# Kernel tuning notes

Hardware: AMD Instinct MI355X
Metric: run time of the kernel (lower is better)

Reference implementation:

```python
import jax, jax.numpy as jnp
import numpy as np

N, E, D_IN, D_OUT = 100000, 3200000, 128, 128


def setup_inputs() -> dict:
    key = jax.random.key(0)
    ks = jax.random.split(key, 6)
    return {
        "x": jax.random.normal(ks[0], (N, D_IN), dtype=jnp.float32),
        "row": jax.random.randint(ks[1], (E,), 0, N),
        "col": jax.random.randint(ks[2], (E,), 0, N),
        "W0": jax.random.normal(ks[3], (D_OUT, D_IN), dtype=jnp.float32) * (1.0 / np.sqrt(D_IN)),
        "b0": jnp.zeros((D_OUT,), jnp.float32),
        "W1": jax.random.normal(ks[4], (D_OUT, D_IN), dtype=jnp.float32) * (1.0 / np.sqrt(D_IN)),
        "b1": jnp.zeros((D_OUT,), jnp.float32),
        "att": jax.random.normal(ks[5], (2 * D_OUT,), dtype=jnp.float32) * 0.1,
        "scale0": jnp.ones((D_OUT,), jnp.float32),
        "offset0": jnp.zeros((D_OUT,), jnp.float32),
        "scale1": jnp.ones((D_OUT,), jnp.float32),
        "offset1": jnp.zeros((D_OUT,), jnp.float32),
    }


def _norm(f, scale, offset):
    # per-node normalization over feature dim (bias='norm' branch)
    m = jnp.mean(f, axis=1, keepdims=True)
    v = jnp.var(f, axis=1, keepdims=True) + 1e-9
    return (f - m) * scale * jax.lax.rsqrt(v) + offset


def reference(x, row, col, W0, b0, W1, b1, att, scale0, offset0, scale1, offset1):
    d = W0.shape[0]
    # order-0 (self) and order-1 (neighbor) feature transforms, act='relu'
    h0 = jax.nn.relu(x @ W0.T + b0)  # [N, d]
    h1 = jax.nn.relu(x @ W1.T + b1)  # [N, d]
    # unnormalized GAT attention (no softmax), LeakyReLU(0.2)
    a_self = jax.nn.leaky_relu(h0 @ att[:d], negative_slope=0.2)   # [N]
    a_neigh = jax.nn.leaky_relu(h1 @ att[d:], negative_slope=0.2)  # [N]
    e = a_self[row] + a_neigh[col]                                 # [E]
    # SpMM: out[i] = sum_{(i,j) in edges} e_ij * h1[j]
    agg = jax.ops.segment_sum(e[:, None] * h1[col], row, num_segments=h0.shape[0])
    # batch-norm style normalization per head, then mean-aggregate over orders
    out = _norm(h0, scale0, offset0) + _norm(agg, scale1, offset1)
    return out
```

## Files before the change

### kernel.cpp

```cpp
#include <hip/hip_runtime.h>
#include <hip/hip_bf16.h>

constexpr int D = 128;
constexpr int BUCKET_SHIFT = 6;
constexpr int BUCKET_CAP_LOG2 = 12;
constexpr int BUCKET_CAP = 1 << BUCKET_CAP_LOG2;
constexpr int SEG_SHIFT = 13;
constexpr int NSEG = 13;
constexpr int BINS_PER_BUCKET = 4 * NSEG * 16;
constexpr int BINS_PER_WAVE = NSEG * 16;
constexpr int ROWSTRIDE = 130;
typedef __hip_bfloat16 bf16;
typedef __attribute__((ext_vector_type(8))) short bf16x8;
typedef __attribute__((ext_vector_type(4))) float f32x4;

__device__ __forceinline__ short f2b(float f) {
  bf16 h = __float2bfloat16(f);
  return *reinterpret_cast<short*>(&h);
}

__global__ void k_cvtW(const float* __restrict__ W0, const float* __restrict__ W1,
                       short* __restrict__ Wb0, short* __restrict__ Wb1)
{
  int i = blockIdx.x * 256 + threadIdx.x;
  if (i < 16384) Wb0[i] = f2b(W0[i]);
  else if (i < 32768) { int j = i - 16384; Wb1[j] = f2b(W1[j]); }
}

__global__ __launch_bounds__(256) void k_gemm(
    const float* __restrict__ x,
    const short* __restrict__ Wb0, const float* __restrict__ b0,
    const short* __restrict__ Wb1, const float* __restrict__ b1,
    const float* __restrict__ att,
    float* __restrict__ h0, bf16* __restrict__ h1b,
    float* __restrict__ a_self, float* __restrict__ a_neigh, int N)
{
  const int t = threadIdx.x;
  const int wv = t >> 6;
  const int l = t & 63;
  const int fb = blockIdx.y;
  const int nbase = blockIdx.x * 64 + wv * 16;
  const int lm = l & 15;
  const int lk = l >> 4;

  const short* __restrict__ W    = fb ? Wb1 : Wb0;
  const float* __restrict__ bias = fb ? b1 : b0;
  const float* __restrict__ attp = att + fb * 128;

  f32x4 acc[8];
#pragma unroll
  for (int i = 0; i < 8; ++i) acc[i] = (f32x4){0.f, 0.f, 0.f, 0.f};

  const int node_a = nbase + lm;
  const bool okA = node_a < N;
  const float* xrow = x + (size_t)node_a * D + lk * 8;

#pragma unroll
  for (int ks = 0; ks < 4; ++ks) {
    float4 a0, a1;
    if (okA) {
      a0 = *reinterpret_cast<const float4*>(xrow + ks * 32);
      a1 = *reinterpret_cast<const float4*>(xrow + ks * 32 + 4);
    } else {
      a0 = make_float4(0.f, 0.f, 0.f, 0.f);
      a1 = a0;
    }
    bf16x8 af;
    af[0] = f2b(a0.x); af[1] = f2b(a0.y); af[2] = f2b(a0.z); af[3] = f2b(a0.w);
    af[4] = f2b(a1.x); af[5] = f2b(a1.y); af[6] = f2b(a1.z); af[7] = f2b(a1.w);
#pragma unroll
    for (int nt = 0; nt < 8; ++nt) {
      const bf16x8 bfr = *reinterpret_cast<const bf16x8*>(
          W + (size_t)(nt * 16 + lm) * D + ks * 32 + lk * 8);
      acc[nt] = __builtin_amdgcn_mfma_f32_16x16x32_bf16(af, bfr, acc[nt], 0, 0, 0);
    }
  }

  float pd[4] = {0.f, 0.f, 0.f, 0.f};
#pragma unroll
  for (int nt = 0; nt < 8; ++nt) {
    const int f = nt * 16 + lm;
    const float bv = bias[f];
    const float av = attp[f];
#pragma unroll
    for (int j = 0; j < 4; ++j) {
      const float r = fmaxf(acc[nt][j] + bv, 0.f);
      pd[j] = fmaf(r, av, pd[j]);
      const int ng = nbase + lk * 4 + j;
      if (ng < N) {
        if (fb == 0) h0[(size_t)ng * D + f] = r;
        else         h1b[(size_t)ng * D + f] = __float2bfloat16(r);
      }
    }
  }
#pragma unroll
  for (int m2 = 1; m2 < 16; m2 <<= 1) {
    pd[0] += __shfl_xor(pd[0], m2, 16);
    pd[1] += __shfl_xor(pd[1], m2, 16);
    pd[2] += __shfl_xor(pd[2], m2, 16);
    pd[3] += __shfl_xor(pd[3], m2, 16);
  }
  if (lm == 0) {
    float* __restrict__ adest = fb ? a_neigh : a_self;
#pragma unroll
    for (int j = 0; j < 4; ++j) {
      const int ng = nbase + lk * 4 + j;
      if (ng < N) adest[ng] = pd[j];
    }
  }
}

__global__ __launch_bounds__(512) void k_binA(
    const int* __restrict__ row, const int* __restrict__ col,
    int* __restrict__ bukCnt, unsigned* __restrict__ buf1, int E, int NBUK)
{
  constexpr int EPB = 16384;
  __shared__ int hist[1600];
  __shared__ int base[1600];
  const int t = threadIdx.x;
  const int e0 = blockIdx.x * EPB;
  const int e1 = min(e0 + EPB, E);

  for (int i = t; i < NBUK; i += 512) hist[i] = 0;
  __syncthreads();
  for (int e = e0 + t; e < e1; e += 512)
    atomicAdd(&hist[row[e] >> BUCKET_SHIFT], 1);
  __syncthreads();
  for (int bk = t; bk < NBUK; bk += 512) {
    int c = hist[bk];
    base[bk] = (c > 0) ? atomicAdd(&bukCnt[bk], c) : 0;
  }
  __syncthreads();
  for (int i = t; i < NBUK; i += 512) hist[i] = 0;
  __syncthreads();
  for (int e = e0 + t; e < e1; e += 512) {
    int r = row[e];
    int c = col[e];
    int bk = r >> BUCKET_SHIFT;
    int pos = base[bk] + atomicAdd(&hist[bk], 1);
    if (pos < BUCKET_CAP)
      buf1[((size_t)bk << BUCKET_CAP_LOG2) + pos] =
          ((unsigned)c << BUCKET_SHIFT) | (unsigned)(r & 63);
  }
}

__global__ __launch_bounds__(1024) void k_scanB(
    const int* __restrict__ bukCnt, int* __restrict__ bukBase,
    int* __restrict__ runs, int NBUK)
{
  __shared__ int sd[1024];
  __shared__ int carry;
  const int t = threadIdx.x;
  if (t == 0) carry = 0;
  __syncthreads();
  for (int r = 0; r * 1024 < NBUK; ++r) {
    const int idx = r * 1024 + t;
    const int v = (idx < NBUK) ? min(bukCnt[idx], BUCKET_CAP) : 0;
    sd[t] = v;
    __syncthreads();
    for (int d2 = 1; d2 < 1024; d2 <<= 1) {
      int o = (t >= d2) ? sd[t - d2] : 0;
      __syncthreads();
      sd[t] += o;
      __syncthreads();
    }
    const int c0 = carry;
    if (idx < NBUK) bukBase[idx] = c0 + sd[t] - v;
    __syncthreads();
    if (t == 1023) carry = c0 + sd[1023];
    __syncthreads();
  }
  if (t == 0) runs[(size_t)NBUK * BINS_PER_BUCKET] = carry;
}

__global__ __launch_bounds__(256) void k_fine(
    const unsigned* __restrict__ buf1,
    const int* __restrict__ bukCnt, const int* __restrict__ bukBase,
    const float* __restrict__ a_self, const float* __restrict__ a_neigh,
    int* __restrict__ runs, int2* __restrict__ colS2, int N)
{
  __shared__ int lhist[BINS_PER_BUCKET], labs[BINS_PER_BUCKET], lcur[BINS_PER_BUCKET];
  __shared__ float asF[64];
  __shared__ int sd[256];
  const int b = blockIdx.x;
  const int t = threadIdx.x;
  const int n = min(bukCnt[b], BUCKET_CAP);
  const unsigned* src = buf1 + ((size_t)b << BUCKET_CAP_LOG2);
  const int rstart = b << BUCKET_SHIFT;

  for (int i = t; i < BINS_PER_BUCKET; i += 256) { lhist[i] = 0; lcur[i] = 0; }
  if (t < 64) {
    float v = (rstart + t < N) ? a_self[rstart + t] : 0.f;
    asF[t] = v > 0.f ? v : 0.2f * v;
  }
  __syncthreads();
  for (int i = t; i < n; i += 256) {
    unsigned e = src[i];
    int r = e & 63, c = e >> BUCKET_SHIFT;
    int bin = (((r >> 4) * NSEG) + (c >> SEG_SHIFT)) * 16 + (r & 15);
    atomicAdd(&lhist[bin], 1);
  }
  __syncthreads();
  int v[4], s = 0;
  const int bin0 = t * 4;
#pragma unroll
  for (int i = 0; i < 4; ++i) {
    v[i] = (bin0 + i < BINS_PER_BUCKET) ? lhist[bin0 + i] : 0;
    s += v[i];
  }
  sd[t] = s;
  __syncthreads();
  for (int d2 = 1; d2 < 256; d2 <<= 1) {
    int o = (t >= d2) ? sd[t - d2] : 0;
    __syncthreads();
    sd[t] += o;
    __syncthreads();
  }
  int excl = sd[t] - s;
  const int gb = bukBase[b];
#pragma unroll
  for (int i = 0; i < 4; ++i) {
    if (bin0 + i < BINS_PER_BUCKET) {
      labs[bin0 + i] = gb + excl;
      runs[(size_t)b * BINS_PER_BUCKET + bin0 + i] = gb + excl;
    }
    excl += v[i];
  }
  __syncthreads();
  for (int i = t; i < n; i += 256) {
    unsigned e = src[i];
    int r = e & 63, c = e >> BUCKET_SHIFT;
    int bin = (((r >> 4) * NSEG) + (c >> SEG_SHIFT)) * 16 + (r & 15);
    int pos = labs[bin] + atomicAdd(&lcur[bin], 1);
    float an = a_neigh[c];
    an = an > 0.f ? an : 0.2f * an;
    colS2[pos] = make_int2((c << 8) | r, __float_as_int(asF[r] + an));
  }
}

__global__ __launch_bounds__(256) void k_agg(
    const float* __restrict__ h0, const bf16* __restrict__ h1b,
    const int* __restrict__ runs, const int2* __restrict__ colS2,
    const float* __restrict__ scale0, const float* __restrict__ offset0,
    const float* __restrict__ scale1, const float* __restrict__ offset1,
    float* __restrict__ out, int N)
{
  __shared__ float aggL[64 * ROWSTRIDE];
  __shared__ int wb[5];
  __shared__ int2 je[4][64];
  const int b = blockIdx.x;
  const int t = threadIdx.x;
  const int w = t >> 6, l = t & 63;
  const int rbase = b << 6;

  for (int i = t; i < 64 * ROWSTRIDE; i += 256) aggL[i] = 0.f;
  if (t < 5) wb[t] = runs[(size_t)b * BINS_PER_BUCKET + (size_t)t * BINS_PER_WAVE];
  __syncthreads();

  const char* h1c = reinterpret_cast<const char*>(h1b) + l * 4;
  int2* jw = je[w];
  float acc0 = 0.f, acc1 = 0.f;
  int curRow = -1;

  auto flush = [&]() {
    float* pp = &aggL[curRow * ROWSTRIDE + 2 * l];
    const float2 o = *reinterpret_cast<const float2*>(pp);
    *reinterpret_cast<float2*>(pp) = make_float2(o.x + acc0, o.y + acc1);
  };
  auto proc = [&](int2 q, unsigned u) {
    const int r_ = q.x & 63;
    if (r_ != curRow) {
      if (curRow >= 0) flush();
      acc0 = 0.f; acc1 = 0.f; curRow = r_;
    }
    const float wg = __int_as_float(q.y);
    acc0 = fmaf(wg, __uint_as_float(u << 16), acc0);
    acc1 = fmaf(wg, __uint_as_float(u & 0xffff0000u), acc1);
  };
  auto ld = [&](int2 q) -> unsigned {
    return *reinterpret_cast<const unsigned*>(
        h1c + (size_t)((unsigned)q.x & 0xFFFFFF00u));
  };

  const int wbeg = wb[w];
  const int wend = wb[w + 1];

  if (wbeg < wend) {
    const int last = wend - 1;
    int2 P = colS2[min(wbeg + l, last)];

    int cur = wbeg;
    while (cur < wend) {
      const int m = min(64, wend - cur);
      if (l < m) jw[l] = P;
      const int2 Pn = colS2[min(cur + 64 + l, last)];

      int k = 0;
      for (; k + 16 <= m; k += 16) {
        int2 q[16]; unsigned u[16];
#pragma unroll
        for (int i = 0; i < 16; ++i) q[i] = jw[k + i];
#pragma unroll
        for (int i = 0; i < 16; ++i) u[i] = ld(q[i]);
#pragma unroll
        for (int i = 0; i < 16; ++i) proc(q[i], u[i]);
      }
      for (; k + 4 <= m; k += 4) {
        const int2 q0 = jw[k], q1 = jw[k + 1], q2 = jw[k + 2], q3 = jw[k + 3];
        const unsigned u0 = ld(q0), u1 = ld(q1), u2 = ld(q2), u3 = ld(q3);
        proc(q0, u0); proc(q1, u1); proc(q2, u2); proc(q3, u3);
      }
      for (; k < m; ++k) {
        const int2 q = jw[k];
        proc(q, ld(q));
      }
      P = Pn;
      cur += m;
    }
    if (curRow >= 0) flush();
  }
  __syncthreads();

  const float2 sc0 = *reinterpret_cast<const float2*>(&scale0[2 * l]);
  const float2 of0 = *reinterpret_cast<const float2*>(&offset0[2 * l]);
  const float2 sc1 = *reinterpret_cast<const float2*>(&scale1[2 * l]);
  const float2 of1 = *reinterpret_cast<const float2*>(&offset1[2 * l]);
  const float inv = 1.0f / 128.0f;
  for (int i = 0; i < 16; ++i) {
    const int node = rbase + (w << 4) + i;
    if (node >= N) break;
    const float2 hv = *reinterpret_cast<const float2*>(&h0[(size_t)node * D + 2 * l]);
    const float2 av = *reinterpret_cast<const float2*>(
        &aggL[((w << 4) + i) * ROWSTRIDE + 2 * l]);
    float sh = hv.x + hv.y, qh = hv.x * hv.x + hv.y * hv.y;
    float sa = av.x + av.y, qa = av.x * av.x + av.y * av.y;
#pragma unroll
    for (int o = 32; o; o >>= 1) {
      sh += __shfl_xor(sh, o, 64); qh += __shfl_xor(qh, o, 64);
      sa += __shfl_xor(sa, o, 64); qa += __shfl_xor(qa, o, 64);
    }
    const float m0 = sh * inv, v0 = qh * inv - m0 * m0 + 1e-9f;
    const float m1 = sa * inv, v1 = qa * inv - m1 * m1 + 1e-9f;
    const float r0 = rsqrtf(v0), r1 = rsqrtf(v1);
    float2 o2;
    o2.x = (hv.x - m0) * sc0.x * r0 + of0.x + (av.x - m1) * sc1.x * r1 + of1.x;
    o2.y = (hv.y - m0) * sc0.y * r0 + of0.y + (av.y - m1) * sc1.y * r1 + of1.y;
    *reinterpret_cast<float2*>(&out[(size_t)node * D + 2 * l]) = o2;
  }
}

extern "C" void kernel_launch(void* const* d_in, const int* in_sizes, int n_in,
                              void* d_out, int out_size, void* d_ws, size_t ws_size,
                              hipStream_t stream)
{
  const float* x       = (const float*)d_in[0];
  const int*   row     = (const int*)d_in[1];
  const int*   col     = (const int*)d_in[2];
  const float* W0      = (const float*)d_in[3];
  const float* b0      = (const float*)d_in[4];
  const float* W1      = (const float*)d_in[5];
  const float* b1      = (const float*)d_in[6];
  const float* att     = (const float*)d_in[7];
  const float* scale0  = (const float*)d_in[8];
  const float* offset0 = (const float*)d_in[9];
  const float* scale1  = (const float*)d_in[10];
  const float* offset1 = (const float*)d_in[11];

  const int N = in_sizes[0] / D;
  const int E = in_sizes[1];
  const int NBUK = (N + 63) >> BUCKET_SHIFT;

  char* ws = (char*)d_ws;
  size_t off = 0;
  auto alloc = [&](size_t bytes) -> void* {
    void* p = ws + off;
    off += (bytes + 511) & ~size_t(511);
    return p;
  };

  float*    h0      = (float*)d_out;
  bf16*     h1b     = (bf16*)alloc((size_t)N * D * sizeof(bf16));
  float*    a_self  = (float*)alloc((size_t)N * sizeof(float));
  float*    a_neigh = (float*)alloc((size_t)N * sizeof(float));
  short*    Wb0     = (short*)alloc(16384 * sizeof(short));
  short*    Wb1     = (short*)alloc(16384 * sizeof(short));
  int*      bukCnt  = (int*)alloc((size_t)NBUK * sizeof(int));
  int*      bukBase = (int*)alloc((size_t)NBUK * sizeof(int));
  int*      runsT   = (int*)alloc(((size_t)NBUK * BINS_PER_BUCKET + 1) * sizeof(int));
  unsigned* buf1    = (unsigned*)alloc(((size_t)NBUK << BUCKET_CAP_LOG2) * sizeof(unsigned));
  int2*     colS2   = (int2*)alloc((size_t)E * sizeof(int2));

  hipMemsetAsync(bukCnt, 0, (size_t)NBUK * sizeof(int), stream);

  k_cvtW<<<128, 256, 0, stream>>>(W0, W1, Wb0, Wb1);
  dim3 ggrid((N + 63) / 64, 2);
  k_gemm<<<ggrid, 256, 0, stream>>>(x, Wb0, b0, Wb1, b1, att, h0, h1b,
                                    a_self, a_neigh, N);
  const int NBLKA = (E + 16383) / 16384;
  k_binA<<<NBLKA, 512, 0, stream>>>(row, col, bukCnt, buf1, E, NBUK);
  k_scanB<<<1, 1024, 0, stream>>>(bukCnt, bukBase, runsT, NBUK);
  k_fine<<<NBUK, 256, 0, stream>>>(buf1, bukCnt, bukBase, a_self, a_neigh,
                                   runsT, colS2, N);
  k_agg<<<NBUK, 256, 0, stream>>>(h0, h1b, runsT, colS2,
                                  scale0, offset0, scale1, offset1,
                                  (float*)d_out, N);
}
```

Before: 292.1 us.

## Fold bucket scan into k_fine and load edges directly in k_agg

Removes the single-block k_scanB launch. Each k_fine block now computes its own global base by summing the counts of all preceding buckets, a redundant O(NBUK) read per block (about 1563 buckets). The per-bin run table becomes a compact 5-entry-per-bucket table of wave boundaries. k_agg drops its LDS staging of edges and loads colS2 entries directly, relying on uniform scalar/broadcast loads via readfirstlane bounds. This trades a serialized launch and LDS traffic for redundant prefix reads and possibly less load pipelining.

```diff
diff --git a/kernel.cpp b/kernel.cpp
--- a/kernel.cpp
+++ b/kernel.cpp
@@ -144,56 +144,40 @@
   }
 }
 
-__global__ __launch_bounds__(1024) void k_scanB(
-    const int* __restrict__ bukCnt, int* __restrict__ bukBase,
-    int* __restrict__ runs, int NBUK)
-{
-  __shared__ int sd[1024];
-  __shared__ int carry;
-  const int t = threadIdx.x;
-  if (t == 0) carry = 0;
-  __syncthreads();
-  for (int r = 0; r * 1024 < NBUK; ++r) {
-    const int idx = r * 1024 + t;
-    const int v = (idx < NBUK) ? min(bukCnt[idx], BUCKET_CAP) : 0;
-    sd[t] = v;
-    __syncthreads();
-    for (int d2 = 1; d2 < 1024; d2 <<= 1) {
-      int o = (t >= d2) ? sd[t - d2] : 0;
-      __syncthreads();
-      sd[t] += o;
-      __syncthreads();
-    }
-    const int c0 = carry;
-    if (idx < NBUK) bukBase[idx] = c0 + sd[t] - v;
-    __syncthreads();
-    if (t == 1023) carry = c0 + sd[1023];
-    __syncthreads();
-  }
-  if (t == 0) runs[(size_t)NBUK * BINS_PER_BUCKET] = carry;
-}
-
 __global__ __launch_bounds__(256) void k_fine(
     const unsigned* __restrict__ buf1,
-    const int* __restrict__ bukCnt, const int* __restrict__ bukBase,
+    const int* __restrict__ bukCnt,
     const float* __restrict__ a_self, const float* __restrict__ a_neigh,
-    int* __restrict__ runs, int2* __restrict__ colS2, int N)
+    int* __restrict__ runsW, int2* __restrict__ colS2, int N)
 {
   __shared__ int lhist[BINS_PER_BUCKET], labs[BINS_PER_BUCKET], lcur[BINS_PER_BUCKET];
   __shared__ float asF[64];
   __shared__ int sd[256];
+  __shared__ int gbS;
   const int b = blockIdx.x;
   const int t = threadIdx.x;
   const int n = min(bukCnt[b], BUCKET_CAP);
   const unsigned* src = buf1 + ((size_t)b << BUCKET_CAP_LOG2);
   const int rstart = b << BUCKET_SHIFT;
 
+  int pre = 0;
+  for (int i = t; i < b; i += 256) pre += min(bukCnt[i], BUCKET_CAP);
+  sd[t] = pre;
+  __syncthreads();
+  for (int d2 = 128; d2 > 0; d2 >>= 1) {
+    if (t < d2) sd[t] += sd[t + d2];
+    __syncthreads();
+  }
+  if (t == 0) gbS = sd[0];
+
   for (int i = t; i < BINS_PER_BUCKET; i += 256) { lhist[i] = 0; lcur[i] = 0; }
   if (t < 64) {
     float v = (rstart + t < N) ? a_self[rstart + t] : 0.f;
     asF[t] = v > 0.f ? v : 0.2f * v;
   }
   __syncthreads();
+  const int gb = gbS;
+
   for (int i = t; i < n; i += 256) {
     unsigned e = src[i];
     int r = e & 63, c = e >> BUCKET_SHIFT;
@@ -217,16 +201,14 @@
     __syncthreads();
   }
   int excl = sd[t] - s;
-  const int gb = bukBase[b];
 #pragma unroll
   for (int i = 0; i < 4; ++i) {
-    if (bin0 + i < BINS_PER_BUCKET) {
-      labs[bin0 + i] = gb + excl;
-      runs[(size_t)b * BINS_PER_BUCKET + bin0 + i] = gb + excl;
-    }
+    if (bin0 + i < BINS_PER_BUCKET) labs[bin0 + i] = gb + excl;
     excl += v[i];
   }
   __syncthreads();
+  if (t < 4) runsW[b * 5 + t] = labs[t * BINS_PER_WAVE];
+  else if (t == 4) runsW[b * 5 + 4] = gb + n;
   for (int i = t; i < n; i += 256) {
     unsigned e = src[i];
     int r = e & 63, c = e >> BUCKET_SHIFT;
@@ -240,25 +222,23 @@
 
 __global__ __launch_bounds__(256) void k_agg(
     const float* __restrict__ h0, const bf16* __restrict__ h1b,
-    const int* __restrict__ runs, const int2* __restrict__ colS2,
+    const int* __restrict__ runsW, const int2* __restrict__ colS2,
     const float* __restrict__ scale0, const float* __restrict__ offset0,
     const float* __restrict__ scale1, const float* __restrict__ offset1,
     float* __restrict__ out, int N)
 {
   __shared__ float aggL[64 * ROWSTRIDE];
   __shared__ int wb[5];
-  __shared__ int2 je[4][64];
   const int b = blockIdx.x;
   const int t = threadIdx.x;
   const int w = t >> 6, l = t & 63;
   const int rbase = b << 6;
 
   for (int i = t; i < 64 * ROWSTRIDE; i += 256) aggL[i] = 0.f;
-  if (t < 5) wb[t] = runs[(size_t)b * BINS_PER_BUCKET + (size_t)t * BINS_PER_WAVE];
+  if (t < 5) wb[t] = runsW[b * 5 + t];
   __syncthreads();
 
   const char* h1c = reinterpret_cast<const char*>(h1b) + l * 4;
-  int2* jw = je[w];
   float acc0 = 0.f, acc1 = 0.f;
   int curRow = -1;
 
@@ -282,43 +262,33 @@
         h1c + (size_t)((unsigned)q.x & 0xFFFFFF00u));
   };
 
-  const int wbeg = wb[w];
-  const int wend = wb[w + 1];
-
-  if (wbeg < wend) {
-    const int last = wend - 1;
-    int2 P = colS2[min(wbeg + l, last)];
-
-    int cur = wbeg;
-    while (cur < wend) {
-      const int m = min(64, wend - cur);
-      if (l < m) jw[l] = P;
-      const int2 Pn = colS2[min(cur + 64 + l, last)];
-
-      int k = 0;
-      for (; k + 16 <= m; k += 16) {
-        int2 q[16]; unsigned u[16];
-#pragma unroll
-        for (int i = 0; i < 16; ++i) q[i] = jw[k + i];
-#pragma unroll
-        for (int i = 0; i < 16; ++i) u[i] = ld(q[i]);
-#pragma unroll
-        for (int i = 0; i < 16; ++i) proc(q[i], u[i]);
-      }
-      for (; k + 4 <= m; k += 4) {
-        const int2 q0 = jw[k], q1 = jw[k + 1], q2 = jw[k + 2], q3 = jw[k + 3];
-        const unsigned u0 = ld(q0), u1 = ld(q1), u2 = ld(q2), u3 = ld(q3);
-        proc(q0, u0); proc(q1, u1); proc(q2, u2); proc(q3, u3);
-      }
-      for (; k < m; ++k) {
-        const int2 q = jw[k];
-        proc(q, ld(q));
-      }
-      P = Pn;
-      cur += m;
-    }
-    if (curRow >= 0) flush();
-  }
+  const int wbeg = __builtin_amdgcn_readfirstlane(wb[w]);
+  const int wend = __builtin_amdgcn_readfirstlane(wb[w + 1]);
+
+  int k = wbeg;
+  for (; k + 16 <= wend; k += 16) {
+    int2 q[16]; unsigned u[16];
+#pragma unroll
+    for (int i = 0; i < 16; ++i) q[i] = colS2[k + i];
+#pragma unroll
+    for (int i = 0; i < 16; ++i) u[i] = ld(q[i]);
+#pragma unroll
+    for (int i = 0; i < 16; ++i) proc(q[i], u[i]);
+  }
+  for (; k + 4 <= wend; k += 4) {
+    int2 q[4]; unsigned u[4];
+#pragma unroll
+    for (int i = 0; i < 4; ++i) q[i] = colS2[k + i];
+#pragma unroll
+    for (int i = 0; i < 4; ++i) u[i] = ld(q[i]);
+#pragma unroll
+    for (int i = 0; i < 4; ++i) proc(q[i], u[i]);
+  }
+  for (; k < wend; ++k) {
+    const int2 q = colS2[k];
+    proc(q, ld(q));
+  }
+  if (curRow >= 0) flush();
   __syncthreads();
 
   const float2 sc0 = *reinterpret_cast<const float2*>(&scale0[2 * l]);
@@ -385,8 +355,7 @@
   short*    Wb0     = (short*)alloc(16384 * sizeof(short));
   short*    Wb1     = (short*)alloc(16384 * sizeof(short));
   int*      bukCnt  = (int*)alloc((size_t)NBUK * sizeof(int));
-  int*      bukBase = (int*)alloc((size_t)NBUK * sizeof(int));
-  int*      runsT   = (int*)alloc(((size_t)NBUK * BINS_PER_BUCKET + 1) * sizeof(int));
+  int*      runsW   = (int*)alloc((size_t)NBUK * 5 * sizeof(int));
   unsigned* buf1    = (unsigned*)alloc(((size_t)NBUK << BUCKET_CAP_LOG2) * sizeof(unsigned));
   int2*     colS2   = (int2*)alloc((size_t)E * sizeof(int2));
 
@@ -398,10 +367,9 @@
                                     a_self, a_neigh, N);
   const int NBLKA = (E + 16383) / 16384;
   k_binA<<<NBLKA, 512, 0, stream>>>(row, col, bukCnt, buf1, E, NBUK);
-  k_scanB<<<1, 1024, 0, stream>>>(bukCnt, bukBase, runsT, NBUK);
-  k_fine<<<NBUK, 256, 0, stream>>>(buf1, bukCnt, bukBase, a_self, a_neigh,
-                                   runsT, colS2, N);
-  k_agg<<<NBUK, 256, 0, stream>>>(h0, h1b, runsT, colS2,
+  k_fine<<<NBUK, 256, 0, stream>>>(buf1, bukCnt, a_self, a_neigh,
+                                   runsW, colS2, N);
+  k_agg<<<NBUK, 256, 0, stream>>>(h0, h1b, runsW, colS2,
                                   scale0, offset0, scale1, offset1,
                                   (float*)d_out, N);
 }
```

Measured after the change: 285.6 us. -2.2%, faster.
